# Kernel optimization log

Measured on AMD Instinct MI355X. Metric: run time of the kernel, lower is better.

The kernel has to match this reference:

```python
import jax, jax.numpy as jnp
import numpy as np

B, N, MODES, WIDTH = 4, 8192, 12, 32
TWO = 2 * MODES  # 24
M_TOT = TWO * (TWO - 1)  # 552


def setup_inputs() -> dict:
    key = jax.random.key(0)
    ks = jax.random.split(key, 12)
    scale = 1.0 / (WIDTH * WIDTH)
    x = jax.random.uniform(ks[0], (B, N, 2), jnp.float32)
    fc0_w = jax.random.normal(ks[1], (2, WIDTH), jnp.float32) * 0.1
    fc0_b = jax.random.normal(ks[2], (WIDTH,), jnp.float32) * 0.05
    # 4 layers x {weights1, weights2}, stored as real/imag pairs (torch.rand cfloat ~ U[0,1)+1j*U[0,1))
    spec_w = jax.random.uniform(ks[3], (4, 2, WIDTH, WIDTH, MODES, MODES, 2), jnp.float32) * scale
    conv_w = jax.random.normal(ks[4], (4, WIDTH, WIDTH), jnp.float32) * 0.1  # Conv1d k=1 -> [O,I]
    conv_b = jax.random.normal(ks[5], (4, WIDTH), jnp.float32) * 0.05
    fc1_w = jax.random.normal(ks[6], (WIDTH, 128), jnp.float32) * 0.1
    fc1_b = jax.random.normal(ks[7], (128,), jnp.float32) * 0.05
    fc2_w = jax.random.normal(ks[8], (128, 1), jnp.float32) * 0.1
    fc2_b = jax.random.normal(ks[9], (1,), jnp.float32) * 0.05
    return {"x": x, "fc0_w": fc0_w, "fc0_b": fc0_b, "spec_w": spec_w,
            "conv_w": conv_w, "conv_b": conv_b, "fc1_w": fc1_w, "fc1_b": fc1_b,
            "fc2_w": fc2_w, "fc2_b": fc2_b}


def _vft_matrices(xp, yp):
    # xp, yp: [B, N], already min-shifted and scaled to [0, 6.28]
    kx = jnp.concatenate([jnp.arange(MODES), jnp.arange(-MODES, 0)]).astype(jnp.float32)       # [24]
    ky = jnp.concatenate([jnp.arange(MODES), jnp.arange(-(MODES - 1), 0)]).astype(jnp.float32)  # [23]
    Xm = kx[None, :, None] * xp[:, None, :]  # [B,24,N]
    Ym = ky[None, :, None] * yp[:, None, :]  # [B,23,N]
    # torch: X repeat(1,23,1) tiles blocks; Y repeat(1,1,24).reshape interleaves -> row j*24+i = X[i]+Y[j]
    phase = jnp.tile(Xm, (1, TWO - 1, 1)) + jnp.repeat(Ym, TWO, axis=1)  # [B,552,N]
    V_fwd = jnp.exp(-1j * phase)                    # [B,552,N] complex64
    V_inv = jnp.conj(V_fwd).transpose(0, 2, 1)      # [B,N,552]
    return V_fwd, V_inv


def _spectral_conv(h, V_fwd, V_inv, w1, w2):
    # h: [B,C,N] real; w1,w2: [C,C,M,M] complex
    b, c, n = h.shape
    # forward Vandermonde transform: bmm(V_fwd, h^T) then permute -> [B,C,552]
    x_ft = jnp.einsum('bmn,bnc->bcm', V_fwd, h.astype(jnp.complex64).transpose(0, 2, 1))
    x_ft = x_ft.reshape(b, c, TWO, TWO - 1)
    top = jnp.einsum('bixy,ioxy->boxy', x_ft[:, :, :MODES, :MODES], w1)
    bot = jnp.einsum('bixy,ioxy->boxy', x_ft[:, :, -MODES:, :MODES], w2)
    out_ft = jnp.zeros((b, WIDTH, TWO, MODES), jnp.complex64)
    out_ft = out_ft.at[:, :, :MODES, :MODES].set(top)
    out_ft = out_ft.at[:, :, -MODES:, :MODES].set(bot)
    x_ft = out_ft.reshape(b, WIDTH, 2 * MODES * MODES)  # [B,C,288]
    # conjugate-symmetric completion (flip over last two dims, as in source)
    x_ft2 = jnp.conj(jnp.flip(x_ft[..., TWO:], axis=(-2, -1)))  # [B,C,264]
    x_ft = jnp.concatenate([x_ft, x_ft2], axis=-1)  # [B,C,552]
    out = jnp.einsum('bnm,bmc->bcn', V_inv, x_ft.transpose(0, 2, 1))  # [B,C,N]
    return (out / n * 2).real


def reference(x, fc0_w, fc0_b, spec_w, conv_w, conv_b, fc1_w, fc1_b, fc2_w, fc2_b):
    gelu = lambda t: jax.nn.gelu(t, approximate=False)
    # VFT mutates x in-place by subtracting global mins (view semantics in torch)
    xp = x[:, :, 0] - jnp.min(x[:, :, 0])
    yp = x[:, :, 1] - jnp.min(x[:, :, 1])
    x_in = jnp.stack([xp, yp], axis=-1)  # what fc0 actually sees
    V_fwd, V_inv = _vft_matrices(xp * 6.28 / jnp.max(xp), yp * 6.28 / jnp.max(yp))
    h = (x_in @ fc0_w + fc0_b).transpose(0, 2, 1)  # [B,C,N]
    for l in range(4):
        w1 = spec_w[l, 0, ..., 0] + 1j * spec_w[l, 0, ..., 1]
        w2 = spec_w[l, 1, ..., 0] + 1j * spec_w[l, 1, ..., 1]
        x1 = _spectral_conv(h, V_fwd, V_inv, w1, w2)
        x2 = jnp.einsum('bin,oi->bon', h, conv_w[l]) + conv_b[l][None, :, None]
        h = x1 + x2
        if l < 3:
            h = gelu(h)
    h = h.transpose(0, 2, 1)  # [B,N,C]
    h = gelu(h @ fc1_w + fc1_b)
    return h @ fc2_w + fc2_b  # [B,N,1]
```

## Files before the change

kernel.cpp:

```cpp
#include <hip/hip_runtime.h>
#include <cmath>

#define NB 4
#define NN 8192
#define CH 32

typedef short short8 __attribute__((ext_vector_type(8)));
typedef float floatx4 __attribute__((ext_vector_type(4)));
typedef unsigned short ushort_t;

__device__ __forceinline__ unsigned short f2b(float f){
  unsigned u = __float_as_uint(f);
  u = u + 0x7FFFu + ((u >> 16) & 1u);
  return (unsigned short)(u >> 16);
}
__device__ __forceinline__ float b2f(unsigned short h){
  return __uint_as_float(((unsigned)h) << 16);
}
__device__ __forceinline__ float gelu_f(float v){
  return 0.5f * v * (1.0f + erff(v * 0.70710678118654752440f));
}
__device__ __forceinline__ int repk(int t){
  int j = t / 24, i = t - j * 24;
  if(j == 0)  return (i <= 12) ? i : -1;
  if(j <= 11) return 13 + (j - 1) * 24 + i;
  return (i == 12) ? 277 + (j - 12) : -1;
}
__device__ __forceinline__ int partner(int t){
  int j = t / 24, i = t - j * 24;
  return ((23 - j) % 23) * 24 + ((24 - i) % 24);
}
__device__ __forceinline__ int repT(int k){
  if(k < 13) return k;
  if(k < 277){ int m = k - 13; return (m / 24 + 1) * 24 + (m % 24); }
  return (k - 277 + 12) * 24 + 12;
}

__global__ __launch_bounds__(256) void k_pre(const float* __restrict__ spec,
    float2* __restrict__ wt, const float* __restrict__ x, float4* __restrict__ pmm,
    const float* __restrict__ fc1w, ushort_t* __restrict__ WB)
{
  const int tid = threadIdx.x;
  if(blockIdx.x < 128){
    int g = blockIdx.x * 256 + tid;
    float a = x[(size_t)g * 2], b = x[(size_t)g * 2 + 1];
    float mn0 = a, mx0 = a, mn1 = b, mx1 = b;
    for(int off = 32; off > 0; off >>= 1){
      mn0 = fminf(mn0, __shfl_down(mn0, off));
      mx0 = fmaxf(mx0, __shfl_down(mx0, off));
      mn1 = fminf(mn1, __shfl_down(mn1, off));
      mx1 = fmaxf(mx1, __shfl_down(mx1, off));
    }
    __shared__ float4 wp[4];
    if((tid & 63) == 0) wp[tid >> 6] = make_float4(mn0, mn1, mx0, mx1);
    __syncthreads();
    if(tid == 0){
      float4 r = wp[0];
      for(int i2 = 1; i2 < 4; ++i2){
        float4 v = wp[i2];
        r.x = fminf(r.x, v.x); r.y = fminf(r.y, v.y);
        r.z = fmaxf(r.z, v.z); r.w = fmaxf(r.w, v.w);
      }
      pmm[blockIdx.x] = r;
    }
  } else if(blockIdx.x < 4736){
    int g = (blockIdx.x - 128) * 256 + tid;
    int o  = g & 31;
    int i  = (g >> 5) & 31;
    int rest = g >> 10;
    int pq = rest % 144;
    int ls = rest / 144;
    wt[g] = ((const float2*)spec)[(((size_t)(ls * 32 + i) * 32 + o) * 144 + pq)];
  } else {
    for(int s = tid; s < 512; s += 256){
      int jt = s >> 6, l = s & 63;
      int c = l & 15, qq = l >> 4;
      #pragma unroll
      for(int e = 0; e < 8; ++e){
        float wv = fc1w[(qq * 8 + e) * 128 + jt * 16 + c];
        ushort_t hi = f2b(wv);
        WB[(jt * 64 + l) * 8 + e] = hi;
        WB[4096 + (jt * 64 + l) * 8 + e] = f2b(wv - b2f(hi));
      }
    }
  }
}

__global__ __launch_bounds__(256) void k_vbuild(const float* __restrict__ x,
    const float4* __restrict__ pmm, const float* __restrict__ fw,
    const float* __restrict__ fb, ushort_t* __restrict__ AF, ushort_t* __restrict__ VTF,
    float* __restrict__ h, ushort_t* __restrict__ hb)
{
  __shared__ ushort_t lds1[32 * 584];
  __shared__ float4 mmv;
  const int tid = threadIdx.x;
  if(tid < 64){
    float4 a = pmm[tid], c = pmm[tid + 64];
    float mn0 = fminf(a.x, c.x), mn1 = fminf(a.y, c.y);
    float mx0 = fmaxf(a.z, c.z), mx1 = fmaxf(a.w, c.w);
    for(int off = 32; off > 0; off >>= 1){
      mn0 = fminf(mn0, __shfl_down(mn0, off));
      mn1 = fminf(mn1, __shfl_down(mn1, off));
      mx0 = fmaxf(mx0, __shfl_down(mx0, off));
      mx1 = fmaxf(mx1, __shfl_down(mx1, off));
    }
    if(tid == 0) mmv = make_float4(mn0, mn1, mx0, mx1);
  }
  __syncthreads();
  const int nl = tid & 31, part = tid >> 5;
  const int b = blockIdx.x >> 8;
  const int nblk = blockIdx.x & 255;
  const int n = nblk * 32 + nl;
  float mn0 = mmv.x, mn1 = mmv.y, mx0 = mmv.z, mx1 = mmv.w;
  float x0 = x[(size_t)(b * NN + n) * 2]     - mn0;
  float x1 = x[(size_t)(b * NN + n) * 2 + 1] - mn1;
  float sp = x0 * (6.28f / (mx0 - mn0));
  float sq = x1 * (6.28f / (mx1 - mn1));
  float cx, sx, cy, sy;
  sincosf(sp, &sx, &cx);
  sincosf(sq, &sy, &cy);
  int j0 = part * 3;
  int j1 = (j0 + 3 < 23) ? j0 + 3 : 23;
  float ky0 = (j0 < 12) ? (float)j0 : (float)(j0 - 23);
  float cb, sb;
  sincosf(ky0 * sq, &sb, &cb);
  for(int j = j0; j < j1; ++j){
    float ca = 1.0f, sa = 0.0f;
    #pragma unroll
    for(int i = 0; i < 24; ++i){
      float vr = ca * cb - sa * sb;
      float vi = -(sa * cb + ca * sb);
      int t = j * 24 + i;
      int k = repk(t);
      if(k >= 0){
        lds1[nl * 584 + k]       = f2b(vr);
        lds1[nl * 584 + 288 + k] = f2b(vi);
      }
      float cn = ca * cx - sa * sx;
      float sn = sa * cx + ca * sx;
      if(i == 11) sn = -sn;
      ca = cn; sa = sn;
    }
    float cbn = cb * cy - sb * sy;
    float sbn = sb * cy + cb * sy;
    cb = cbn; sb = sbn;
  }
  __syncthreads();
  #pragma unroll
  for(int r = 0; r < 9; ++r){
    int c = tid + 256 * r;
    int t16 = c / 1152;
    int c2 = c - t16 * 1152;
    int kk = c2 >> 6;
    int rem = c2 & 63;
    int q = rem >> 4, n15 = rem & 15;
    short8 v = *(const short8*)(lds1 + (t16 * 16 + n15) * 584 + kk * 32 + q * 8);
    *(short8*)(VTF + ((size_t)((b * 512 + nblk * 2 + t16) * 18 + kk)) * 512
               + (q * 16 + n15) * 8) = v;
  }
  #pragma unroll
  for(int r = 0; r < 9; ++r){
    int c = tid + 256 * r;
    int st = c >> 6;
    int rem = c & 63;
    int q = rem >> 4, srow = rem & 15;
    int sg = st * 16 + srow;
    int s = (sg < 288) ? sg : sg - 288;
    int sinh_ = (sg >= 288);
    int p2 = s / 12, qq = s - p2 * 12;
    int t = p2 * 23 + qq;
    int k = repk(t);
    unsigned short flip = 0;
    if(k < 0){ k = repk(partner(t)); if(sinh_) flip = 0x8000; }
    int col = sinh_ ? 288 + k : k;
    ushort_t tmp[8];
    #pragma unroll
    for(int e = 0; e < 8; ++e)
      tmp[e] = lds1[(q * 8 + e) * 584 + col] ^ flip;
    *(short8*)(AF + ((size_t)((b * 36 + st) * 256 + nblk)) * 512
               + (q * 16 + srow) * 8) = *(short8*)tmp;
  }
  #pragma unroll
  for(int rr = 0; rr < 4; ++rr){
    int c2 = (tid >> 5) + rr * 8;
    float v = fb[c2] + x0 * fw[c2] + x1 * fw[32 + c2];
    size_t idx = (size_t)(b * CH + c2) * NN + n;
    h[idx] = v; hb[idx] = f2b(v);
  }
}

__global__ __launch_bounds__(256) void k_fwd(const ushort_t* __restrict__ AF,
    const ushort_t* __restrict__ hb, float* __restrict__ xp)
{
  const int stp = blockIdx.x;
  const int ks = blockIdx.y;
  const int b  = blockIdx.z;
  const int w = threadIdx.x >> 6;
  const int lane = threadIdx.x & 63;
  const int row = lane & 15;
  const int q = lane >> 4;
  const int st0 = stp * 2;
  const size_t abase0 = ((size_t)(b * 36 + st0) * 256) * 512 + (q * 16 + row) * 8;
  const size_t abase1 = abase0 + (size_t)256 * 512;
  const size_t hb0 = (size_t)(b * CH + row) * NN;
  const size_t hb1 = hb0 + (size_t)16 * NN;
  floatx4 aA0 = {0.f,0.f,0.f,0.f}, aA1 = {0.f,0.f,0.f,0.f};
  floatx4 aB0 = {0.f,0.f,0.f,0.f}, aB1 = {0.f,0.f,0.f,0.f};
  #pragma unroll
  for(int kk = 0; kk < 8; ++kk){
    int g = ks * 32 + w * 8 + kk;
    short8 A0 = *(const short8*)(AF + abase0 + (size_t)g * 512);
    short8 A1 = *(const short8*)(AF + abase1 + (size_t)g * 512);
    int nn2 = g * 32 + q * 8;
    short8 B0 = *(const short8*)(hb + hb0 + nn2);
    short8 B1 = *(const short8*)(hb + hb1 + nn2);
    aA0 = __builtin_amdgcn_mfma_f32_16x16x32_bf16(A0, B0, aA0, 0, 0, 0);
    aA1 = __builtin_amdgcn_mfma_f32_16x16x32_bf16(A0, B1, aA1, 0, 0, 0);
    aB0 = __builtin_amdgcn_mfma_f32_16x16x32_bf16(A1, B0, aB0, 0, 0, 0);
    aB1 = __builtin_amdgcn_mfma_f32_16x16x32_bf16(A1, B1, aB1, 0, 0, 0);
  }
  __shared__ float red[4 * 512];
  const int e = threadIdx.x;
  #pragma unroll
  for(int r = 0; r < 4; ++r){
    int rrow = q * 4 + r;
    red[w * 512 + rrow * 32 + row]      = aA0[r];
    red[w * 512 + rrow * 32 + 16 + row] = aA1[r];
  }
  __syncthreads();
  {
    float v0 = red[e] + red[512 + e] + red[1024 + e] + red[1536 + e];
    float v1 = red[e + 256] + red[512 + e + 256] + red[1024 + e + 256] + red[1536 + e + 256];
    size_t base = ((size_t)(ks * NB + b) * 576 + st0 * 16) * 32;
    xp[base + e] = v0;
    xp[base + e + 256] = v1;
  }
  __syncthreads();
  #pragma unroll
  for(int r = 0; r < 4; ++r){
    int rrow = q * 4 + r;
    red[w * 512 + rrow * 32 + row]      = aB0[r];
    red[w * 512 + rrow * 32 + 16 + row] = aB1[r];
  }
  __syncthreads();
  {
    float v0 = red[e] + red[512 + e] + red[1024 + e] + red[1536 + e];
    float v1 = red[e + 256] + red[512 + e + 256] + red[1024 + e + 256] + red[1536 + e + 256];
    size_t base = ((size_t)(ks * NB + b) * 576 + (st0 + 1) * 16) * 32;
    xp[base + e] = v0;
    xp[base + e + 256] = v1;
  }
}

__global__ __launch_bounds__(256) void k_mixg(const float* __restrict__ xp,
    const float2* __restrict__ wt, ushort_t* __restrict__ ghi, ushort_t* __restrict__ glo,
    int layer)
{
  const int w = threadIdx.x >> 6;
  const int lane = threadIdx.x & 63;
  const int k = blockIdx.x * 4 + w;
  const int b = blockIdx.y;
  const int t = repT(k);
  const int j = t / 24, i = t - j * 24;
  const int u = partner(t);
  const bool unpaired = (i == 12) || (u == t);
  const int idxT = (t < 288) ? t : 575 - t;  const bool cfT = (t >= 288);
  const int idxU = (u < 288) ? u : 575 - u;  const bool cfU = (u >= 288);
  __shared__ float Xs[4][2][64];
  const int o = lane & 31, half = lane >> 5;
  #pragma unroll
  for(int m = 0; m < 2; ++m){
    int idx = m ? idxU : idxT;
    int rrow = half ? 288 + idx : idx;
    float s = 0.f;
    #pragma unroll
    for(int ks = 0; ks < 8; ++ks)
      s += xp[((size_t)(ks * NB + b) * 576 + rrow) * 32 + o];
    Xs[w][m][half * 32 + o] = s;
  }
  __syncthreads();
  float Fr[2], Fi[2];
  #pragma unroll
  for(int m = 0; m < 2; ++m){
    int idx = m ? idxU : idxT;
    int p2 = idx / 12, qq = idx - p2 * 12;
    int sel = (p2 < 12) ? 0 : 1;
    int pq = (p2 % 12) * 12 + qq;
    const float2* wb = wt + ((size_t)((layer * 2 + sel) * 144 + pq)) * 1024;
    int i0 = half * 16;
    float fr = 0.f, fi = 0.f;
    #pragma unroll
    for(int ii = 0; ii < 16; ++ii){
      int i2 = i0 + ii;
      float xr = Xs[w][m][i2], xi = Xs[w][m][32 + i2];
      float2 wv = wb[i2 * 32 + o];
      fr += xr * wv.x - xi * wv.y;
      fi += xr * wv.y + xi * wv.x;
    }
    fr += __shfl_down(fr, 32);
    fi += __shfl_down(fi, 32);
    Fr[m] = fr; Fi[m] = fi;
  }
  const int c = lane & 31;
  const int srcT = cfT ? 31 - c : c;
  const int srcU = cfU ? 31 - c : c;
  float fax = __shfl(Fr[0], srcT);
  float fay = __shfl(Fi[0], srcT);
  float fbx = __shfl(Fr[1], srcU);
  float fby = __shfl(Fi[1], srcU);
  if(lane < 32){
    float gr = fax;
    float gi = cfT ? -fay : fay;
    if(!unpaired){
      gr += fbx;
      gi -= (cfU ? -fby : fby);
    }
    unsigned short hr = f2b(gr); float lr = gr - b2f(hr);
    unsigned short hi2 = f2b(gi); float li = gi - b2f(hi2);
    size_t base = (size_t)(b * CH + c) * 576;
    ghi[base + k] = hr;          ghi[base + 288 + k] = hi2;
    glo[base + k] = f2b(lr);     glo[base + 288 + k] = f2b(li);
  }
}

template<int LAST>
__global__ __launch_bounds__(512, 2) void k_inv(const ushort_t* __restrict__ VTF,
    const ushort_t* __restrict__ ghi, const ushort_t* __restrict__ glo,
    const float* __restrict__ hfull, const float* __restrict__ cw,
    const float* __restrict__ cbias, float* __restrict__ hout,
    ushort_t* __restrict__ houtb, int layer,
    const float* __restrict__ w1, const float* __restrict__ b1,
    const float* __restrict__ w2, const float* __restrict__ b2,
    float* __restrict__ out, const ushort_t* __restrict__ WBg)
{
  __shared__ ushort_t GH[32][584];
  __shared__ ushort_t GL[32][584];
  __shared__ float hTc[32][129];
  __shared__ float Wl[1024];
  __shared__ float Bl[32];
  const int tid = threadIdx.x;
  const int b = blockIdx.y;
  const int n0 = blockIdx.x * 128;
  for(int idx = tid; idx < 2304; idx += 512){
    int ch = idx / 72, g8 = (idx - ch * 72) * 8;
    size_t src = (size_t)(b * CH + ch) * 576 + g8;
    *(short8*)&GH[ch][g8] = *(const short8*)(ghi + src);
    *(short8*)&GL[ch][g8] = *(const short8*)(glo + src);
  }
  {
    int ch = tid >> 4, grp = tid & 15;
    const float* src = hfull + (size_t)(b * CH + ch) * NN + n0 + grp * 8;
    float4 v0 = *(const float4*)src;
    float4 v1 = *(const float4*)(src + 4);
    int p = grp * 8;
    hTc[ch][p + 0] = v0.x; hTc[ch][p + 1] = v0.y;
    hTc[ch][p + 2] = v0.z; hTc[ch][p + 3] = v0.w;
    hTc[ch][p + 4] = v1.x; hTc[ch][p + 5] = v1.y;
    hTc[ch][p + 6] = v1.z; hTc[ch][p + 7] = v1.w;
  }
  for(int idx = tid; idx < 1024; idx += 512)
    Wl[(idx & 31) * 32 + (idx >> 5)] = cw[layer * 1024 + idx];
  if(tid < 32) Bl[tid] = cbias[layer * 32 + tid];
  __syncthreads();
  const int lane = tid & 63;
  const int w = tid >> 6;
  const int row = lane & 15;
  const int q = lane >> 4;
  const int nloc = w * 16 + row;
  const int n = n0 + nloc;
  const int n16 = blockIdx.x * 8 + w;
  const ushort_t* vb = VTF + ((size_t)(b * 512 + n16) * 18) * 512 + (q * 16 + row) * 8;
  const int ko = q * 8;
  floatx4 a0h = {0.f,0.f,0.f,0.f}, a0l = {0.f,0.f,0.f,0.f};
  floatx4 a1h = {0.f,0.f,0.f,0.f}, a1l = {0.f,0.f,0.f,0.f};
  #pragma unroll
  for(int kk = 0; kk < 18; ++kk){
    short8 Bv  = *(const short8*)(vb + (size_t)kk * 512);
    short8 Ah0 = *(const short8*)&GH[row][ko + kk * 32];
    short8 Al0 = *(const short8*)&GL[row][ko + kk * 32];
    short8 Ah1 = *(const short8*)&GH[16 + row][ko + kk * 32];
    short8 Al1 = *(const short8*)&GL[16 + row][ko + kk * 32];
    a0h = __builtin_amdgcn_mfma_f32_16x16x32_bf16(Ah0, Bv, a0h, 0, 0, 0);
    a0l = __builtin_amdgcn_mfma_f32_16x16x32_bf16(Al0, Bv, a0l, 0, 0, 0);
    a1h = __builtin_amdgcn_mfma_f32_16x16x32_bf16(Ah1, Bv, a1h, 0, 0, 0);
    a1l = __builtin_amdgcn_mfma_f32_16x16x32_bf16(Al1, Bv, a1l, 0, 0, 0);
  }
  floatx4 acc0 = a0h + a0l;
  floatx4 acc1 = a1h + a1l;
  float acc2[8];
  {
    const int c0 = q * 4;
    #pragma unroll
    for(int r = 0; r < 4; ++r){ acc2[r] = Bl[c0 + r]; acc2[4 + r] = Bl[16 + c0 + r]; }
    #pragma unroll
    for(int i = 0; i < CH; ++i){
      float hv = hTc[i][nloc];
      float4 wv0 = *(const float4*)&Wl[i * 32 + c0];
      float4 wv1 = *(const float4*)&Wl[i * 32 + 16 + c0];
      acc2[0] = fmaf(hv, wv0.x, acc2[0]);
      acc2[1] = fmaf(hv, wv0.y, acc2[1]);
      acc2[2] = fmaf(hv, wv0.z, acc2[2]);
      acc2[3] = fmaf(hv, wv0.w, acc2[3]);
      acc2[4] = fmaf(hv, wv1.x, acc2[4]);
      acc2[5] = fmaf(hv, wv1.y, acc2[5]);
      acc2[6] = fmaf(hv, wv1.z, acc2[6]);
      acc2[7] = fmaf(hv, wv1.w, acc2[7]);
    }
  }
  const float sc = 2.0f / 8192.0f;
  if constexpr(!LAST){
    #pragma unroll
    for(int r = 0; r < 4; ++r){
      int c = q * 4 + r;
      float v0 = gelu_f(acc0[r] * sc + acc2[r]);
      size_t idx0 = (size_t)(b * CH + c) * NN + n;
      hout[idx0] = v0; houtb[idx0] = f2b(v0);
      float v1 = gelu_f(acc1[r] * sc + acc2[4 + r]);
      size_t idx1 = (size_t)(b * CH + 16 + c) * NN + n;
      hout[idx1] = v1; houtb[idx1] = f2b(v1);
    }
  } else {
    __shared__ ushort_t hHi[128][32];
    __shared__ ushort_t hLo[128][32];
    __shared__ ushort_t WBs[8192];
    __shared__ float b1s[128], w2s[128];
    {
      ushort_t H0[4], L0[4], H1[4], L1[4];
      #pragma unroll
      for(int r = 0; r < 4; ++r){
        float v0 = acc0[r] * sc + acc2[r];
        H0[r] = f2b(v0); L0[r] = f2b(v0 - b2f(H0[r]));
        float v1 = acc1[r] * sc + acc2[4 + r];
        H1[r] = f2b(v1); L1[r] = f2b(v1 - b2f(H1[r]));
      }
      uint2 u;
      u.x = (unsigned)H0[0] | ((unsigned)H0[1] << 16);
      u.y = (unsigned)H0[2] | ((unsigned)H0[3] << 16);
      *(uint2*)&hHi[nloc][q * 4] = u;
      u.x = (unsigned)L0[0] | ((unsigned)L0[1] << 16);
      u.y = (unsigned)L0[2] | ((unsigned)L0[3] << 16);
      *(uint2*)&hLo[nloc][q * 4] = u;
      u.x = (unsigned)H1[0] | ((unsigned)H1[1] << 16);
      u.y = (unsigned)H1[2] | ((unsigned)H1[3] << 16);
      *(uint2*)&hHi[nloc][16 + q * 4] = u;
      u.x = (unsigned)L1[0] | ((unsigned)L1[1] << 16);
      u.y = (unsigned)L1[2] | ((unsigned)L1[3] << 16);
      *(uint2*)&hLo[nloc][16 + q * 4] = u;
    }
    for(int idx = tid; idx < 1024; idx += 512)
      ((short8*)WBs)[idx] = ((const short8*)WBg)[idx];
    if(tid < 128){ b1s[tid] = b1[tid]; w2s[tid] = w2[tid]; }
    __syncthreads();
    const int cl = lane & 15;
    short8 Ahi = *(const short8*)&hHi[w * 16 + cl][ko];
    short8 Alo = *(const short8*)&hLo[w * 16 + cl][ko];
    const float b2v = b2[0];
    float S0 = 0.f, S1 = 0.f, S2 = 0.f, S3 = 0.f;
    #pragma unroll
    for(int jt = 0; jt < 8; ++jt){
      short8 Bhi = *(const short8*)(WBs + (jt * 64 + lane) * 8);
      short8 Blo = *(const short8*)(WBs + 4096 + (jt * 64 + lane) * 8);
      floatx4 acc = {0.f, 0.f, 0.f, 0.f};
      acc = __builtin_amdgcn_mfma_f32_16x16x32_bf16(Ahi, Bhi, acc, 0, 0, 0);
      acc = __builtin_amdgcn_mfma_f32_16x16x32_bf16(Alo, Bhi, acc, 0, 0, 0);
      acc = __builtin_amdgcn_mfma_f32_16x16x32_bf16(Ahi, Blo, acc, 0, 0, 0);
      float bv = b1s[jt * 16 + cl], wv = w2s[jt * 16 + cl];
      S0 = fmaf(gelu_f(acc[0] + bv), wv, S0);
      S1 = fmaf(gelu_f(acc[1] + bv), wv, S1);
      S2 = fmaf(gelu_f(acc[2] + bv), wv, S2);
      S3 = fmaf(gelu_f(acc[3] + bv), wv, S3);
    }
    #pragma unroll
    for(int off = 8; off; off >>= 1){
      S0 += __shfl_xor(S0, off, 16);
      S1 += __shfl_xor(S1, off, 16);
      S2 += __shfl_xor(S2, off, 16);
      S3 += __shfl_xor(S3, off, 16);
    }
    if(cl == 0){
      size_t ob = (size_t)b * NN + n0 + w * 16 + q * 4;
      out[ob + 0] = S0 + b2v;
      out[ob + 1] = S1 + b2v;
      out[ob + 2] = S2 + b2v;
      out[ob + 3] = S3 + b2v;
    }
  }
}

extern "C" void kernel_launch(void* const* d_in, const int* in_sizes, int n_in,
                              void* d_out, int out_size, void* d_ws, size_t ws_size,
                              hipStream_t stream)
{
  const float* x      = (const float*)d_in[0];
  const float* fc0_w  = (const float*)d_in[1];
  const float* fc0_b  = (const float*)d_in[2];
  const float* spec_w = (const float*)d_in[3];
  const float* conv_w = (const float*)d_in[4];
  const float* conv_b = (const float*)d_in[5];
  const float* fc1_w  = (const float*)d_in[6];
  const float* fc1_b  = (const float*)d_in[7];
  const float* fc2_w  = (const float*)d_in[8];
  const float* fc2_b  = (const float*)d_in[9];
  float* out = (float*)d_out;

  char* w = (char*)d_ws;
  const size_t OFF_PMM  = 0;
  const size_t OFF_WT   = 4096;
  const size_t OFF_AF   = OFF_WT  + 9437184;
  const size_t OFF_VTF  = OFF_AF  + 37748736;
  const size_t OFF_H0   = OFF_VTF + 37748736;
  const size_t OFF_H1   = OFF_H0  + 4194304;
  const size_t OFF_H0B  = OFF_H1  + 4194304;
  const size_t OFF_H1B  = OFF_H0B + 2097152;
  const size_t OFF_XP   = OFF_H1B + 2097152;
  const size_t OFF_GHI  = OFF_XP  + 2359296;
  const size_t OFF_GLO  = OFF_GHI + 147456;
  const size_t OFF_WB   = OFF_GLO + 147456;

  float4* pmm    = (float4*)(w + OFF_PMM);
  float2* wt     = (float2*)(w + OFF_WT);
  ushort_t* AF   = (ushort_t*)(w + OFF_AF);
  ushort_t* VTF  = (ushort_t*)(w + OFF_VTF);
  float* hbuf[2]     = { (float*)(w + OFF_H0), (float*)(w + OFF_H1) };
  ushort_t* hbufb[2] = { (ushort_t*)(w + OFF_H0B), (ushort_t*)(w + OFF_H1B) };
  float* xp      = (float*)(w + OFF_XP);
  ushort_t* ghi  = (ushort_t*)(w + OFF_GHI);
  ushort_t* glo  = (ushort_t*)(w + OFF_GLO);
  ushort_t* WB   = (ushort_t*)(w + OFF_WB);

  hipLaunchKernelGGL(k_pre, dim3(4737), dim3(256), 0, stream, spec_w, wt, x, pmm,
                     fc1_w, WB);
  hipLaunchKernelGGL(k_vbuild, dim3(1024), dim3(256), 0, stream, x, pmm,
                     fc0_w, fc0_b, AF, VTF, hbuf[0], hbufb[0]);

  for(int l = 0; l < 4; ++l){
    int in = l & 1, outb = 1 - in;
    hipLaunchKernelGGL(k_fwd, dim3(18, 8, NB), dim3(256), 0, stream, AF, hbufb[in], xp);
    hipLaunchKernelGGL(k_mixg, dim3(72, NB), dim3(256), 0, stream, xp, wt, ghi, glo, l);
    if(l < 3)
      hipLaunchKernelGGL(k_inv<0>, dim3(64, NB), dim3(512), 0, stream, VTF, ghi, glo,
                         hbuf[in], conv_w, conv_b, hbuf[outb], hbufb[outb], l,
                         fc1_w, fc1_b, fc2_w, fc2_b, out, WB);
    else
      hipLaunchKernelGGL(k_inv<1>, dim3(64, NB), dim3(512), 0, stream, VTF, ghi, glo,
                         hbuf[in], conv_w, conv_b, hbuf[outb], hbufb[outb], l,
                         fc1_w, fc1_b, fc2_w, fc2_b, out, WB);
  }
  (void)in_sizes; (void)n_in; (void)out_size; (void)ws_size;
}
```

Before: 257.7 us.

## Store bf16 activations in MFMA fragment layout and add transposed LDS copy

The bf16 copy of the activations is now written in a pre-tiled MFMA B-fragment layout, so k_fwd loads each lane's operand as one contiguous 16-byte chunk instead of strided row reads. k_fwd is split to one spectral tile per block, doubling the grid and removing the second reduction pass. k_vbuild keeps an extra swizzled transposed LDS buffer so the AF fragments can be read with a vector load instead of eight scalar LDS reads. The cost is more LDS per k_vbuild block and scattered 2-byte global stores of the bf16 activations in the producer kernels.

```diff
diff --git a/kernel.cpp b/kernel.cpp
--- a/kernel.cpp
+++ b/kernel.cpp
@@ -92,6 +92,7 @@
     float* __restrict__ h, ushort_t* __restrict__ hb)
 {
   __shared__ ushort_t lds1[32 * 584];
+  __shared__ alignas(16) ushort_t ldsT[576 * 32];
   __shared__ float4 mmv;
   const int tid = threadIdx.x;
   if(tid < 64){
@@ -124,6 +125,7 @@
   float ky0 = (j0 < 12) ? (float)j0 : (float)(j0 - 23);
   float cb, sb;
   sincosf(ky0 * sq, &sb, &cb);
+  const int swb = nl >> 3, swe = nl & 7;
   for(int j = j0; j < j1; ++j){
     float ca = 1.0f, sa = 0.0f;
     #pragma unroll
@@ -133,8 +135,12 @@
       int t = j * 24 + i;
       int k = repk(t);
       if(k >= 0){
-        lds1[nl * 584 + k]       = f2b(vr);
-        lds1[nl * 584 + 288 + k] = f2b(vi);
+        ushort_t vhr = f2b(vr), vhi = f2b(vi);
+        lds1[nl * 584 + k]       = vhr;
+        lds1[nl * 584 + 288 + k] = vhi;
+        int c1 = (swb ^ (k & 3)) * 8 + swe;
+        ldsT[k * 32 + c1]         = vhr;
+        ldsT[(288 + k) * 32 + c1] = vhi;
       }
       float cn = ca * cx - sa * sx;
       float sn = sa * cx + ca * sx;
@@ -170,83 +176,64 @@
     int p2 = s / 12, qq = s - p2 * 12;
     int t = p2 * 23 + qq;
     int k = repk(t);
-    unsigned short flip = 0;
-    if(k < 0){ k = repk(partner(t)); if(sinh_) flip = 0x8000; }
+    bool flip = false;
+    if(k < 0){ k = repk(partner(t)); if(sinh_) flip = true; }
     int col = sinh_ ? 288 + k : k;
-    ushort_t tmp[8];
-    #pragma unroll
-    for(int e = 0; e < 8; ++e)
-      tmp[e] = lds1[(q * 8 + e) * 584 + col] ^ flip;
+    short8 v = *(const short8*)(ldsT + col * 32 + ((q ^ (col & 3)) * 8));
+    if(flip){
+      unsigned* up = (unsigned*)&v;
+      up[0] ^= 0x80008000u; up[1] ^= 0x80008000u;
+      up[2] ^= 0x80008000u; up[3] ^= 0x80008000u;
+    }
     *(short8*)(AF + ((size_t)((b * 36 + st) * 256 + nblk)) * 512
-               + (q * 16 + srow) * 8) = *(short8*)tmp;
+               + (q * 16 + srow) * 8) = v;
   }
   #pragma unroll
   for(int rr = 0; rr < 4; ++rr){
-    int c2 = (tid >> 5) + rr * 8;
+    int c2 = part + rr * 8;
     float v = fb[c2] + x0 * fw[c2] + x1 * fw[32 + c2];
-    size_t idx = (size_t)(b * CH + c2) * NN + n;
-    h[idx] = v; hb[idx] = f2b(v);
+    h[(size_t)(b * CH + c2) * NN + n] = v;
+    int half = c2 >> 4, cl = c2 & 15;
+    hb[(((size_t)(b * 2 + half) * 256 + nblk) * 512) + (swb * 16 + cl) * 8 + swe] = f2b(v);
   }
 }
 
 __global__ __launch_bounds__(256) void k_fwd(const ushort_t* __restrict__ AF,
-    const ushort_t* __restrict__ hb, float* __restrict__ xp)
+    const ushort_t* __restrict__ hbB, float* __restrict__ xp)
 {
-  const int stp = blockIdx.x;
+  const int st = blockIdx.x;
   const int ks = blockIdx.y;
   const int b  = blockIdx.z;
   const int w = threadIdx.x >> 6;
   const int lane = threadIdx.x & 63;
   const int row = lane & 15;
   const int q = lane >> 4;
-  const int st0 = stp * 2;
-  const size_t abase0 = ((size_t)(b * 36 + st0) * 256) * 512 + (q * 16 + row) * 8;
-  const size_t abase1 = abase0 + (size_t)256 * 512;
-  const size_t hb0 = (size_t)(b * CH + row) * NN;
-  const size_t hb1 = hb0 + (size_t)16 * NN;
-  floatx4 aA0 = {0.f,0.f,0.f,0.f}, aA1 = {0.f,0.f,0.f,0.f};
-  floatx4 aB0 = {0.f,0.f,0.f,0.f}, aB1 = {0.f,0.f,0.f,0.f};
+  const size_t abase = ((size_t)(b * 36 + st) * 256) * 512 + (q * 16 + row) * 8;
+  const size_t hB0 = ((size_t)(b * 2 + 0) * 256) * 512 + (size_t)lane * 8;
+  const size_t hB1 = ((size_t)(b * 2 + 1) * 256) * 512 + (size_t)lane * 8;
+  floatx4 a0 = {0.f,0.f,0.f,0.f}, a1 = {0.f,0.f,0.f,0.f};
   #pragma unroll
   for(int kk = 0; kk < 8; ++kk){
     int g = ks * 32 + w * 8 + kk;
-    short8 A0 = *(const short8*)(AF + abase0 + (size_t)g * 512);
-    short8 A1 = *(const short8*)(AF + abase1 + (size_t)g * 512);
-    int nn2 = g * 32 + q * 8;
-    short8 B0 = *(const short8*)(hb + hb0 + nn2);
-    short8 B1 = *(const short8*)(hb + hb1 + nn2);
-    aA0 = __builtin_amdgcn_mfma_f32_16x16x32_bf16(A0, B0, aA0, 0, 0, 0);
-    aA1 = __builtin_amdgcn_mfma_f32_16x16x32_bf16(A0, B1, aA1, 0, 0, 0);
-    aB0 = __builtin_amdgcn_mfma_f32_16x16x32_bf16(A1, B0, aB0, 0, 0, 0);
-    aB1 = __builtin_amdgcn_mfma_f32_16x16x32_bf16(A1, B1, aB1, 0, 0, 0);
+    short8 A  = *(const short8*)(AF + abase + (size_t)g * 512);
+    short8 B0 = *(const short8*)(hbB + hB0 + (size_t)g * 512);
+    short8 B1 = *(const short8*)(hbB + hB1 + (size_t)g * 512);
+    a0 = __builtin_amdgcn_mfma_f32_16x16x32_bf16(A, B0, a0, 0, 0, 0);
+    a1 = __builtin_amdgcn_mfma_f32_16x16x32_bf16(A, B1, a1, 0, 0, 0);
   }
   __shared__ float red[4 * 512];
   const int e = threadIdx.x;
   #pragma unroll
   for(int r = 0; r < 4; ++r){
     int rrow = q * 4 + r;
-    red[w * 512 + rrow * 32 + row]      = aA0[r];
-    red[w * 512 + rrow * 32 + 16 + row] = aA1[r];
+    red[w * 512 + rrow * 32 + row]      = a0[r];
+    red[w * 512 + rrow * 32 + 16 + row] = a1[r];
   }
   __syncthreads();
   {
     float v0 = red[e] + red[512 + e] + red[1024 + e] + red[1536 + e];
     float v1 = red[e + 256] + red[512 + e + 256] + red[1024 + e + 256] + red[1536 + e + 256];
-    size_t base = ((size_t)(ks * NB + b) * 576 + st0 * 16) * 32;
-    xp[base + e] = v0;
-    xp[base + e + 256] = v1;
-  }
-  __syncthreads();
-  #pragma unroll
-  for(int r = 0; r < 4; ++r){
-    int rrow = q * 4 + r;
-    red[w * 512 + rrow * 32 + row]      = aB0[r];
-    red[w * 512 + rrow * 32 + 16 + row] = aB1[r];
-  }
-  __syncthreads();
-  {
-    float v0 = red[e] + red[512 + e] + red[1024 + e] + red[1536 + e];
-    float v1 = red[e + 256] + red[512 + e + 256] + red[1024 + e + 256] + red[1536 + e + 256];
-    size_t base = ((size_t)(ks * NB + b) * 576 + (st0 + 1) * 16) * 32;
+    size_t base = ((size_t)(ks * NB + b) * 576 + st * 16) * 32;
     xp[base + e] = v0;
     xp[base + e + 256] = v1;
   }
@@ -409,15 +396,18 @@
   }
   const float sc = 2.0f / 8192.0f;
   if constexpr(!LAST){
+    const int g  = n >> 5;
+    const int qb = (n >> 3) & 3;
+    const int e2 = n & 7;
     #pragma unroll
     for(int r = 0; r < 4; ++r){
       int c = q * 4 + r;
       float v0 = gelu_f(acc0[r] * sc + acc2[r]);
-      size_t idx0 = (size_t)(b * CH + c) * NN + n;
-      hout[idx0] = v0; houtb[idx0] = f2b(v0);
+      hout[(size_t)(b * CH + c) * NN + n] = v0;
+      houtb[(((size_t)(b * 2 + 0) * 256 + g) * 512) + (qb * 16 + c) * 8 + e2] = f2b(v0);
       float v1 = gelu_f(acc1[r] * sc + acc2[4 + r]);
-      size_t idx1 = (size_t)(b * CH + 16 + c) * NN + n;
-      hout[idx1] = v1; houtb[idx1] = f2b(v1);
+      hout[(size_t)(b * CH + 16 + c) * NN + n] = v1;
+      houtb[(((size_t)(b * 2 + 1) * 256 + g) * 512) + (qb * 16 + c) * 8 + e2] = f2b(v1);
     }
   } else {
     __shared__ ushort_t hHi[128][32];
@@ -535,7 +525,7 @@
 
   for(int l = 0; l < 4; ++l){
     int in = l & 1, outb = 1 - in;
-    hipLaunchKernelGGL(k_fwd, dim3(18, 8, NB), dim3(256), 0, stream, AF, hbufb[in], xp);
+    hipLaunchKernelGGL(k_fwd, dim3(36, 8, NB), dim3(256), 0, stream, AF, hbufb[in], xp);
     hipLaunchKernelGGL(k_mixg, dim3(72, NB), dim3(256), 0, stream, xp, wt, ghi, glo, l);
     if(l < 3)
       hipLaunchKernelGGL(k_inv<0>, dim3(64, NB), dim3(512), 0, stream, VTF, ghi, glo,
```

Measured after the change: 273.1 us. 1.06x slower.

## Restructure inverse transform: smaller blocks, split-K across waves, MFMA-fragment G layout

Applied to the files above, without the earlier changes.

The mixing kernel now writes the spectral coefficients (hi/lo bf16) directly in the per-lane MFMA fragment layout, so the inverse kernel can load A operands straight from global/L2 instead of staging 32x576 tiles in LDS. The inverse kernel drops to 32 points per block with 256 threads and 1024 blocks, and splits the K dimension across wave pairs, combining the partial accumulators through a small LDS exchange. The last-layer MLP head also splits the fc1 tiles across the two halves and reduces through shared memory. This cuts LDS footprint and staging time and raises occupancy and block count, at the cost of repeated global reads of G per block and an extra barrier.

```diff
diff --git a/kernel.cpp b/kernel.cpp
--- a/kernel.cpp
+++ b/kernel.cpp
@@ -317,14 +317,17 @@
     }
     unsigned short hr = f2b(gr); float lr = gr - b2f(hr);
     unsigned short hi2 = f2b(gi); float li = gi - b2f(hi2);
-    size_t base = (size_t)(b * CH + c) * 576;
-    ghi[base + k] = hr;          ghi[base + 288 + k] = hi2;
-    glo[base + k] = f2b(lr);     glo[base + 288 + k] = f2b(li);
+    const size_t base = (size_t)b * 18432;
+    int A1 = (k >> 5) * 1024 + ((c >> 4) << 9)
+           + ((((k >> 3) & 3) << 4) + (c & 15)) * 8 + (k & 7);
+    int A2 = A1 + 9 * 1024;
+    ghi[base + A1] = hr;          ghi[base + A2] = hi2;
+    glo[base + A1] = f2b(lr);     glo[base + A2] = f2b(li);
   }
 }
 
 template<int LAST>
-__global__ __launch_bounds__(512, 2) void k_inv(const ushort_t* __restrict__ VTF,
+__global__ __launch_bounds__(256, 4) void k_inv(const ushort_t* __restrict__ VTF,
     const ushort_t* __restrict__ ghi, const ushort_t* __restrict__ glo,
     const float* __restrict__ hfull, const float* __restrict__ cw,
     const float* __restrict__ cbias, float* __restrict__ hout,
@@ -333,133 +336,103 @@
     const float* __restrict__ w2, const float* __restrict__ b2,
     float* __restrict__ out, const ushort_t* __restrict__ WBg)
 {
-  __shared__ ushort_t GH[32][584];
-  __shared__ ushort_t GL[32][584];
-  __shared__ float hTc[32][129];
+  __shared__ floatx4 xch[4][64];
+  __shared__ float hTc[32][33];
   __shared__ float Wl[1024];
   __shared__ float Bl[32];
   const int tid = threadIdx.x;
   const int b = blockIdx.y;
-  const int n0 = blockIdx.x * 128;
-  for(int idx = tid; idx < 2304; idx += 512){
-    int ch = idx / 72, g8 = (idx - ch * 72) * 8;
-    size_t src = (size_t)(b * CH + ch) * 576 + g8;
-    *(short8*)&GH[ch][g8] = *(const short8*)(ghi + src);
-    *(short8*)&GL[ch][g8] = *(const short8*)(glo + src);
-  }
+  const int n0 = blockIdx.x * 32;
   {
-    int ch = tid >> 4, grp = tid & 15;
-    const float* src = hfull + (size_t)(b * CH + ch) * NN + n0 + grp * 8;
-    float4 v0 = *(const float4*)src;
-    float4 v1 = *(const float4*)(src + 4);
-    int p = grp * 8;
-    hTc[ch][p + 0] = v0.x; hTc[ch][p + 1] = v0.y;
-    hTc[ch][p + 2] = v0.z; hTc[ch][p + 3] = v0.w;
-    hTc[ch][p + 4] = v1.x; hTc[ch][p + 5] = v1.y;
-    hTc[ch][p + 6] = v1.z; hTc[ch][p + 7] = v1.w;
-  }
-  for(int idx = tid; idx < 1024; idx += 512)
+    int ch = tid >> 3, grp = tid & 7;
+    float4 v = *(const float4*)(hfull + (size_t)(b * CH + ch) * NN + n0 + grp * 4);
+    int p = grp * 4;
+    hTc[ch][p + 0] = v.x; hTc[ch][p + 1] = v.y;
+    hTc[ch][p + 2] = v.z; hTc[ch][p + 3] = v.w;
+  }
+  for(int idx = tid; idx < 1024; idx += 256)
     Wl[(idx & 31) * 32 + (idx >> 5)] = cw[layer * 1024 + idx];
   if(tid < 32) Bl[tid] = cbias[layer * 32 + tid];
-  __syncthreads();
   const int lane = tid & 63;
   const int w = tid >> 6;
-  const int row = lane & 15;
-  const int q = lane >> 4;
-  const int nloc = w * 16 + row;
-  const int n = n0 + nloc;
-  const int n16 = blockIdx.x * 8 + w;
-  const ushort_t* vb = VTF + ((size_t)(b * 512 + n16) * 18) * 512 + (q * 16 + row) * 8;
-  const int ko = q * 8;
+  const int tl = w >> 1;
+  const int kh = w & 1;
+  const int row = lane & 15, q = lane >> 4;
+  const int n16 = blockIdx.x * 2 + tl;
+  const ushort_t* vb = VTF + ((size_t)(b * 512 + n16) * 18 + kh * 9) * 512 + lane * 8;
+  const ushort_t* gH = ghi + (size_t)b * 18432 + kh * 9 * 1024 + lane * 8;
+  const ushort_t* gL = glo + (size_t)b * 18432 + kh * 9 * 1024 + lane * 8;
   floatx4 a0h = {0.f,0.f,0.f,0.f}, a0l = {0.f,0.f,0.f,0.f};
   floatx4 a1h = {0.f,0.f,0.f,0.f}, a1l = {0.f,0.f,0.f,0.f};
   #pragma unroll
-  for(int kk = 0; kk < 18; ++kk){
-    short8 Bv  = *(const short8*)(vb + (size_t)kk * 512);
-    short8 Ah0 = *(const short8*)&GH[row][ko + kk * 32];
-    short8 Al0 = *(const short8*)&GL[row][ko + kk * 32];
-    short8 Ah1 = *(const short8*)&GH[16 + row][ko + kk * 32];
-    short8 Al1 = *(const short8*)&GL[16 + row][ko + kk * 32];
+  for(int kk = 0; kk < 9; ++kk){
+    short8 Bv  = *(const short8*)(vb + kk * 512);
+    short8 Ah0 = *(const short8*)(gH + kk * 1024);
+    short8 Ah1 = *(const short8*)(gH + kk * 1024 + 512);
+    short8 Al0 = *(const short8*)(gL + kk * 1024);
+    short8 Al1 = *(const short8*)(gL + kk * 1024 + 512);
     a0h = __builtin_amdgcn_mfma_f32_16x16x32_bf16(Ah0, Bv, a0h, 0, 0, 0);
     a0l = __builtin_amdgcn_mfma_f32_16x16x32_bf16(Al0, Bv, a0l, 0, 0, 0);
     a1h = __builtin_amdgcn_mfma_f32_16x16x32_bf16(Ah1, Bv, a1h, 0, 0, 0);
     a1l = __builtin_amdgcn_mfma_f32_16x16x32_bf16(Al1, Bv, a1l, 0, 0, 0);
   }
-  floatx4 acc0 = a0h + a0l;
-  floatx4 acc1 = a1h + a1l;
-  float acc2[8];
-  {
-    const int c0 = q * 4;
-    #pragma unroll
-    for(int r = 0; r < 4; ++r){ acc2[r] = Bl[c0 + r]; acc2[4 + r] = Bl[16 + c0 + r]; }
-    #pragma unroll
-    for(int i = 0; i < CH; ++i){
-      float hv = hTc[i][nloc];
-      float4 wv0 = *(const float4*)&Wl[i * 32 + c0];
-      float4 wv1 = *(const float4*)&Wl[i * 32 + 16 + c0];
-      acc2[0] = fmaf(hv, wv0.x, acc2[0]);
-      acc2[1] = fmaf(hv, wv0.y, acc2[1]);
-      acc2[2] = fmaf(hv, wv0.z, acc2[2]);
-      acc2[3] = fmaf(hv, wv0.w, acc2[3]);
-      acc2[4] = fmaf(hv, wv1.x, acc2[4]);
-      acc2[5] = fmaf(hv, wv1.y, acc2[5]);
-      acc2[6] = fmaf(hv, wv1.z, acc2[6]);
-      acc2[7] = fmaf(hv, wv1.w, acc2[7]);
-    }
+  floatx4 p0 = a0h + a0l;
+  floatx4 p1 = a1h + a1l;
+  xch[w][lane] = kh ? p0 : p1;
+  __syncthreads();
+  floatx4 accF = (kh ? p1 : p0) + xch[tl * 2 + (1 - kh)][lane];
+  const int cb = kh * 16 + q * 4;
+  const int pt = tl * 16 + row;
+  float acc2[4] = { Bl[cb], Bl[cb + 1], Bl[cb + 2], Bl[cb + 3] };
+  #pragma unroll
+  for(int i = 0; i < CH; ++i){
+    float hv = hTc[i][pt];
+    float4 wv = *(const float4*)&Wl[i * 32 + cb];
+    acc2[0] = fmaf(hv, wv.x, acc2[0]);
+    acc2[1] = fmaf(hv, wv.y, acc2[1]);
+    acc2[2] = fmaf(hv, wv.z, acc2[2]);
+    acc2[3] = fmaf(hv, wv.w, acc2[3]);
   }
   const float sc = 2.0f / 8192.0f;
   if constexpr(!LAST){
     #pragma unroll
     for(int r = 0; r < 4; ++r){
-      int c = q * 4 + r;
-      float v0 = gelu_f(acc0[r] * sc + acc2[r]);
-      size_t idx0 = (size_t)(b * CH + c) * NN + n;
-      hout[idx0] = v0; houtb[idx0] = f2b(v0);
-      float v1 = gelu_f(acc1[r] * sc + acc2[4 + r]);
-      size_t idx1 = (size_t)(b * CH + 16 + c) * NN + n;
-      hout[idx1] = v1; houtb[idx1] = f2b(v1);
+      int c = cb + r;
+      float v = gelu_f(accF[r] * sc + acc2[r]);
+      size_t idx = (size_t)(b * CH + c) * NN + n0 + pt;
+      hout[idx] = v; houtb[idx] = f2b(v);
     }
   } else {
-    __shared__ ushort_t hHi[128][32];
-    __shared__ ushort_t hLo[128][32];
-    __shared__ ushort_t WBs[8192];
+    __shared__ ushort_t hHi[32][40];
+    __shared__ ushort_t hLo[32][40];
     __shared__ float b1s[128], w2s[128];
+    __shared__ float part[2][32];
     {
-      ushort_t H0[4], L0[4], H1[4], L1[4];
+      ushort_t H[4], L[4];
       #pragma unroll
       for(int r = 0; r < 4; ++r){
-        float v0 = acc0[r] * sc + acc2[r];
-        H0[r] = f2b(v0); L0[r] = f2b(v0 - b2f(H0[r]));
-        float v1 = acc1[r] * sc + acc2[4 + r];
-        H1[r] = f2b(v1); L1[r] = f2b(v1 - b2f(H1[r]));
+        float v = accF[r] * sc + acc2[r];
+        H[r] = f2b(v); L[r] = f2b(v - b2f(H[r]));
       }
-      uint2 u;
-      u.x = (unsigned)H0[0] | ((unsigned)H0[1] << 16);
-      u.y = (unsigned)H0[2] | ((unsigned)H0[3] << 16);
-      *(uint2*)&hHi[nloc][q * 4] = u;
-      u.x = (unsigned)L0[0] | ((unsigned)L0[1] << 16);
-      u.y = (unsigned)L0[2] | ((unsigned)L0[3] << 16);
-      *(uint2*)&hLo[nloc][q * 4] = u;
-      u.x = (unsigned)H1[0] | ((unsigned)H1[1] << 16);
-      u.y = (unsigned)H1[2] | ((unsigned)H1[3] << 16);
-      *(uint2*)&hHi[nloc][16 + q * 4] = u;
-      u.x = (unsigned)L1[0] | ((unsigned)L1[1] << 16);
-      u.y = (unsigned)L1[2] | ((unsigned)L1[3] << 16);
-      *(uint2*)&hLo[nloc][16 + q * 4] = u;
-    }
-    for(int idx = tid; idx < 1024; idx += 512)
-      ((short8*)WBs)[idx] = ((const short8*)WBg)[idx];
+      uint2 uu;
+      uu.x = (unsigned)H[0] | ((unsigned)H[1] << 16);
+      uu.y = (unsigned)H[2] | ((unsigned)H[3] << 16);
+      *(uint2*)&hHi[pt][cb] = uu;
+      uu.x = (unsigned)L[0] | ((unsigned)L[1] << 16);
+      uu.y = (unsigned)L[2] | ((unsigned)L[3] << 16);
+      *(uint2*)&hLo[pt][cb] = uu;
+    }
     if(tid < 128){ b1s[tid] = b1[tid]; w2s[tid] = w2[tid]; }
     __syncthreads();
-    const int cl = lane & 15;
-    short8 Ahi = *(const short8*)&hHi[w * 16 + cl][ko];
-    short8 Alo = *(const short8*)&hLo[w * 16 + cl][ko];
-    const float b2v = b2[0];
+    const int cl = row;
+    short8 Ahi = *(const short8*)&hHi[tl * 16 + cl][q * 8];
+    short8 Alo = *(const short8*)&hLo[tl * 16 + cl][q * 8];
     float S0 = 0.f, S1 = 0.f, S2 = 0.f, S3 = 0.f;
     #pragma unroll
-    for(int jt = 0; jt < 8; ++jt){
-      short8 Bhi = *(const short8*)(WBs + (jt * 64 + lane) * 8);
-      short8 Blo = *(const short8*)(WBs + 4096 + (jt * 64 + lane) * 8);
+    for(int jt2 = 0; jt2 < 4; ++jt2){
+      int jt = kh * 4 + jt2;
+      short8 Bhi = *(const short8*)(WBg + (jt * 64 + lane) * 8);
+      short8 Blo = *(const short8*)(WBg + 4096 + (jt * 64 + lane) * 8);
       floatx4 acc = {0.f, 0.f, 0.f, 0.f};
       acc = __builtin_amdgcn_mfma_f32_16x16x32_bf16(Ahi, Bhi, acc, 0, 0, 0);
       acc = __builtin_amdgcn_mfma_f32_16x16x32_bf16(Alo, Bhi, acc, 0, 0, 0);
@@ -478,12 +451,15 @@
       S3 += __shfl_xor(S3, off, 16);
     }
     if(cl == 0){
-      size_t ob = (size_t)b * NN + n0 + w * 16 + q * 4;
-      out[ob + 0] = S0 + b2v;
-      out[ob + 1] = S1 + b2v;
-      out[ob + 2] = S2 + b2v;
-      out[ob + 3] = S3 + b2v;
-    }
+      int pb = tl * 16 + q * 4;
+      part[kh][pb + 0] = S0;
+      part[kh][pb + 1] = S1;
+      part[kh][pb + 2] = S2;
+      part[kh][pb + 3] = S3;
+    }
+    __syncthreads();
+    if(tid < 32)
+      out[(size_t)b * NN + n0 + tid] = part[0][tid] + part[1][tid] + b2[0];
   }
 }
 
@@ -538,11 +514,11 @@
     hipLaunchKernelGGL(k_fwd, dim3(18, 8, NB), dim3(256), 0, stream, AF, hbufb[in], xp);
     hipLaunchKernelGGL(k_mixg, dim3(72, NB), dim3(256), 0, stream, xp, wt, ghi, glo, l);
     if(l < 3)
-      hipLaunchKernelGGL(k_inv<0>, dim3(64, NB), dim3(512), 0, stream, VTF, ghi, glo,
+      hipLaunchKernelGGL(k_inv<0>, dim3(256, NB), dim3(256), 0, stream, VTF, ghi, glo,
                          hbuf[in], conv_w, conv_b, hbuf[outb], hbufb[outb], l,
                          fc1_w, fc1_b, fc2_w, fc2_b, out, WB);
     else
-      hipLaunchKernelGGL(k_inv<1>, dim3(64, NB), dim3(512), 0, stream, VTF, ghi, glo,
+      hipLaunchKernelGGL(k_inv<1>, dim3(256, NB), dim3(256), 0, stream, VTF, ghi, glo,
                          hbuf[in], conv_w, conv_b, hbuf[outb], hbufb[outb], l,
                          fc1_w, fc1_b, fc2_w, fc2_b, out, WB);
   }
```

New measurement: 358.3 us. 1.39x slower.
